# Optimization experiments

Hardware: AMD Instinct MI355X
Metric: run time of the kernel (lower is better)

## Reference

```python
import jax, jax.numpy as jnp
import numpy as np

EPS = 1e-6


def smooth(p):
    # smooth_distribution: clamp Bernoulli params away from {0,1}
    return jnp.clip(p, EPS, 1.0 - EPS)


def bern_logprob(p, x):
    # Bernoulli(p).log_prob(x) = x*log(p) + (1-x)*log(1-p)
    return x * jnp.log(p) + (1.0 - x) * jnp.log1p(-p)


def binary_row_reduce(A, b, k):
    # GF(2) Gaussian elimination on [A | b]; A:(k,n) binary float, b:(k,)
    M = jnp.concatenate([A, b[:, None]], axis=1)  # (k, n+1)
    rows = jnp.arange(k)
    for i in range(k):  # k is a small static int (25)
        col = M[:, i]
        cand = jnp.where((rows >= i) & (col > 0.5), rows, k)
        p = jnp.minimum(jnp.min(cand), k - 1)  # pivot row (fallback k-1 if none; prob ~0 for random A)
        ri, rp = M[i], M[p]
        M = M.at[i].set(rp)
        M = M.at[p].set(ri)
        elim = (M[:, i] > 0.5) & (rows != i)
        M = jnp.where(elim[:, None], jnp.mod(M + M[i], 2.0), M)
    return M[:, :-1], M[:, -1]


def compute_term1(logq, logp):
    # stable [sum_s q*log p]/[sum_s q], summed over batch; logq,logp: (S,B)
    m = jnp.max(logq, axis=0)                                  # (B,)
    w = jnp.exp(logq - m)                                      # (S,B)
    neg_num = m + jnp.log(jnp.sum(w * (-logp), axis=0))
    pos_den = m + jnp.log(jnp.sum(w, axis=0))
    return -jnp.sum(jnp.exp(neg_num - pos_den))


def setup_inputs() -> dict:
    key = jax.random.key(0)
    ks = jax.random.split(key, 5)
    nx, nz, B = 2048, 256, 512
    wr = float(np.sqrt(6.0 / (nx + nz)))
    xr = float(np.sqrt(6.0 / nx))
    zr = float(np.sqrt(6.0 / nz))
    U = jax.random.uniform(ks[0], (nz, nx), minval=-wr, maxval=wr)
    V = jax.random.uniform(ks[1], (nx, nz), minval=-wr, maxval=wr)
    x_bias = jax.random.uniform(ks[2], (nx,), minval=-xr, maxval=xr)
    z_bias = jax.random.uniform(ks[3], (nz,), minval=-zr, maxval=zr)
    xin = (jax.random.uniform(ks[4], (B, nx)) < 0.5).astype(jnp.float32)
    return {"xin": xin, "U": U, "V": V, "x_bias": x_bias, "z_bias": z_bias,
            "S": 10, "k": 25, "T": 30}


def reference(xin, U, V, x_bias, z_bias, S, k, T):
    dt = xin.dtype
    key = jax.random.key(42)
    kz, kx, kA, kb = jax.random.split(key, 4)

    # q(z|x) and samples  -------------------------------------------------
    q = smooth(jax.nn.sigmoid(xin @ U.T + z_bias))                     # (B, nz)
    samples_z = (jax.random.uniform(kz, (S,) + q.shape) < q).astype(dt)  # (S,B,nz)
    ps = smooth(jax.nn.sigmoid(jnp.einsum('sbz,xz->sbx', samples_z, V) + x_bias))  # (S,B,nx)
    xouts = (jax.random.uniform(kx, ps.shape) < ps).astype(dt)

    # projected ELBO over T random GF(2) hash constraints ------------------
    nz = U.shape[0]
    A_all = (jax.random.uniform(kA, (T, k, nz)) < 0.5).astype(dt)
    b_all = (jax.random.uniform(kb, (T, k)) < 0.5).astype(dt)
    pz = smooth(jax.nn.sigmoid(z_bias))                                # (nz,)

    def elbo_t(carry, Ab):
        A, b = Ab
        C, bp = binary_row_reduce(A, b, k)                             # (k,nz),(k,)
        proj = jnp.mod(jnp.einsum('sbz,kz->sbk', samples_z[:, :, k:], C[:, k:]) + bp, 2.0)
        sz = samples_z.at[:, :, :k].set(proj)                          # (S,B,nz)
        logq_zi = bern_logprob(q, sz).sum(axis=2)                      # (S,B)
        logp_z = bern_logprob(pz, sz).sum(axis=2)                      # (S,B)
        ps_t = smooth(jax.nn.sigmoid(jnp.einsum('sbz,xz->sbx', sz, V) + x_bias))
        logp_x = bern_logprob(ps_t, xin).sum(axis=2)                   # (S,B)
        logp = logp_z + logp_x
        term2 = compute_term1(logq_zi, logq_zi)
        term1 = compute_term1(logq_zi, logp)
        return carry, term1 - term2

    _, pelbos = jax.lax.scan(elbo_t, 0.0, (A_all, b_all))
    loss = -jnp.mean(pelbos)
    return q, samples_z, ps, xouts, loss
```

## Files before the change

kernel.cpp:

```cpp
#include <hip/hip_runtime.h>
#include <cstdint>

#define NX 2048
#define NZ 256
#define NB 512
#define NS 10
#define NK 25
#define NT 30
#define SBTOT (NS * NB)

#define LOG2E 1.4426950408889634f
#define LN2 0.6931471805599453f

#define OFF_Q 0
#define OFF_SAMP (NB * NZ)
#define OFF_PS (OFF_SAMP + SBTOT * NZ)
#define OFF_XO (OFF_PS + SBTOT * NX)
#define OFF_LOSS (OFF_XO + SBTOT * NX)

typedef unsigned long long ull;
typedef __bf16 bf16x8 __attribute__((ext_vector_type(8)));
typedef float f32x4 __attribute__((ext_vector_type(4)));

__host__ __device__ inline void tf2x32(uint32_t k0, uint32_t k1, uint32_t x0, uint32_t x1,
                                       uint32_t& o0, uint32_t& o1) {
  uint32_t k2 = k0 ^ k1 ^ 0x1BD11BDAu;
  x0 += k0; x1 += k1;
#define TF_R(r) { x0 += x1; x1 = (x1 << (r)) | (x1 >> (32 - (r))); x1 ^= x0; }
  TF_R(13) TF_R(15) TF_R(26) TF_R(6)
  x0 += k1; x1 += k2 + 1u;
  TF_R(17) TF_R(29) TF_R(16) TF_R(24)
  x0 += k2; x1 += k0 + 2u;
  TF_R(13) TF_R(15) TF_R(26) TF_R(6)
  x0 += k0; x1 += k1 + 3u;
  TF_R(17) TF_R(29) TF_R(16) TF_R(24)
  x0 += k1; x1 += k2 + 4u;
  TF_R(13) TF_R(15) TF_R(26) TF_R(6)
  x0 += k2; x1 += k0 + 5u;
#undef TF_R
  o0 = x0; o1 = x1;
}

__device__ inline uint32_t tf_select(uint32_t k0, uint32_t k1, uint32_t i, uint32_t h) {
  bool lo = i < h;
  uint32_t x0 = lo ? i : i - h;
  uint32_t x1 = lo ? i + h : i;
  uint32_t o0, o1;
  tf2x32(k0, k1, x0, x1, o0, o1);
  return lo ? o0 : o1;
}

__device__ inline float tf_uniform(uint32_t k0, uint32_t k1, uint32_t i, uint32_t h) {
  uint32_t r = tf_select(k0, k1, i, h);
  return __uint_as_float(0x3f800000u | (r >> 9)) - 1.0f;
}

__device__ inline float sigclip(float a) {
  float p = 1.0f / (1.0f + __expf(-a));
  return fminf(fmaxf(p, 1e-6f), 1.0f - 1e-6f);
}

__device__ inline ushort f2bf(float f) {
  uint32_t u = __float_as_uint(f);
  return (ushort)((u + 0x7FFFu + ((u >> 16) & 1u)) >> 16);
}

__device__ inline float blockReduceSum256(float v, volatile float* s4) {
#pragma unroll
  for (int o = 32; o > 0; o >>= 1) v += __shfl_down(v, o);
  __syncthreads();
  if ((threadIdx.x & 63) == 0) s4[threadIdx.x >> 6] = v;
  __syncthreads();
  return s4[0] + s4[1] + s4[2] + s4[3];
}

__global__ __launch_bounds__(256) void kP0_prep(const float* __restrict__ V,
                                                const float* __restrict__ U,
                                                const float* __restrict__ xin,
                                                const float* __restrict__ z_bias,
                                                ushort* __restrict__ Vbf,
                                                ushort* __restrict__ Vkpad2,
                                                ushort* __restrict__ Uhi,
                                                ushort* __restrict__ Ulo,
                                                ushort* __restrict__ xinbf,
                                                float* __restrict__ baseq,
                                                float* __restrict__ d_lpz,
                                                float* __restrict__ basepz) {
  __shared__ float red[4];
  int e = blockIdx.x * 256 + threadIdx.x;
  {
    int x = e >> 8, k = e & 255;
    float v = V[e];
    Vbf[e] = f2bf(v);
    if (k < 32) Vkpad2[x * 32 + k] = (k < NK) ? f2bf(v * LOG2E) : (ushort)0;
  }
  {
    float u = U[e];
    ushort hi = f2bf(u);
    Uhi[e] = hi;
    float hv = __uint_as_float((uint32_t)hi << 16);
    Ulo[e] = f2bf(u - hv);
  }
  {
    xinbf[e] = (xin[e] > 0.5f) ? (ushort)0x3F80 : (ushort)0;
    int e2 = e + NX * NZ;
    xinbf[e2] = (xin[e2] > 0.5f) ? (ushort)0x3F80 : (ushort)0;
  }
  if (e < NB) baseq[e] = 0.0f;
  if (blockIdx.x == 0) {
    int z = threadIdx.x;
    float pz = sigclip(z_bias[z]);
    float lp = __logf(pz), l1 = __logf(1.0f - pz);
    d_lpz[z] = lp - l1;
    float s = blockReduceSum256(l1, red);
    if (z == 0) *basepz = s;
  }
}

__global__ __launch_bounds__(256) void kW_signdot(const float* __restrict__ xin,
                                                  const ushort* __restrict__ Vkpad2,
                                                  float* __restrict__ W) {
  __shared__ float wred[4][NK];
  int b = blockIdx.x;
  int tid = threadIdx.x;
  float acc[NK];
#pragma unroll
  for (int j = 0; j < NK; ++j) acc[j] = 0.0f;
#pragma unroll
  for (int i = 0; i < 8; ++i) {
    int x = i * 256 + tid;
    float s = 1.0f - 2.0f * xin[(size_t)b * NX + x];
    const uint4* vp = (const uint4*)(Vkpad2 + (size_t)x * 32);
    uint4 q0 = vp[0], q1 = vp[1], q2 = vp[2], q3 = vp[3];
    uint32_t w[16] = {q0.x, q0.y, q0.z, q0.w, q1.x, q1.y, q1.z, q1.w,
                      q2.x, q2.y, q2.z, q2.w, q3.x, q3.y, q3.z, q3.w};
#pragma unroll
    for (int j = 0; j < NK; ++j) {
      uint32_t wd = w[j >> 1];
      float v = __uint_as_float((j & 1) ? (wd & 0xFFFF0000u) : (wd << 16));
      acc[j] = fmaf(s, v, acc[j]);
    }
  }
#pragma unroll
  for (int j = 0; j < NK; ++j) {
#pragma unroll
    for (int o = 1; o < 64; o <<= 1) acc[j] += __shfl_xor(acc[j], o);
  }
  if ((tid & 63) == 0) {
#pragma unroll
    for (int j = 0; j < NK; ++j) wred[tid >> 6][j] = acc[j];
  }
  __syncthreads();
  if (tid < NK) W[b * 32 + tid] = wred[0][tid] + wred[1][tid] + wred[2][tid] + wred[3][tid];
}

__global__ __launch_bounds__(256) void k1a_mfma(const ushort* __restrict__ xinbf,
                                                const ushort* __restrict__ Uhi,
                                                const ushort* __restrict__ Ulo,
                                                const float* __restrict__ z_bias,
                                                float* __restrict__ outq,
                                                float* __restrict__ d_lq,
                                                float* __restrict__ baseq) {
  __shared__ float red[4][16][17];
  int tid = threadIdx.x;
  int wave = tid >> 6, lane = tid & 63, grp = lane >> 4, col = lane & 15;
  int b0 = (blockIdx.x >> 4) * 16;
  int z0 = (blockIdx.x & 15) * 16;
  f32x4 acc = {0.f, 0.f, 0.f, 0.f};
  const ushort* arow = xinbf + (size_t)(b0 + col) * NX + wave * 512 + grp * 8;
  const ushort* bhr = Uhi + (size_t)(z0 + col) * NX + wave * 512 + grp * 8;
  const ushort* blr = Ulo + (size_t)(z0 + col) * NX + wave * 512 + grp * 8;
#pragma unroll 4
  for (int s = 0; s < 16; ++s) {
    bf16x8 a = *(const bf16x8*)(arow + s * 32);
    bf16x8 bh = *(const bf16x8*)(bhr + s * 32);
    bf16x8 bl = *(const bf16x8*)(blr + s * 32);
    acc = __builtin_amdgcn_mfma_f32_16x16x32_bf16(a, bh, acc, 0, 0, 0);
    acc = __builtin_amdgcn_mfma_f32_16x16x32_bf16(a, bl, acc, 0, 0, 0);
  }
#pragma unroll
  for (int r = 0; r < 4; ++r) red[wave][grp * 4 + r][col] = acc[r];
  __syncthreads();
  int bi = tid >> 4, zi = tid & 15;
  float aa = red[0][bi][zi] + red[1][bi][zi] + red[2][bi][zi] + red[3][bi][zi] + z_bias[z0 + zi];
  int b = b0 + bi, z = z0 + zi;
  float q = sigclip(aa);
  outq[b * NZ + z] = q;
  float lq = __logf(q), l1 = __logf(1.0f - q);
  d_lq[b * NZ + z] = lq - l1;
  float s1 = l1;
#pragma unroll
  for (int o = 1; o < 16; o <<= 1) s1 += __shfl_xor(s1, o);
  if (zi == 0) atomicAdd(&baseq[b], s1);
}

__global__ __launch_bounds__(256) void k2_samples(const float* __restrict__ q,
                                                  const float* __restrict__ d_lq,
                                                  const float* __restrict__ d_lpz,
                                                  float* __restrict__ samp_out,
                                                  ushort* __restrict__ samp16,
                                                  ull* __restrict__ Spack,
                                                  float* __restrict__ qtail,
                                                  float* __restrict__ ptail,
                                                  uint32_t kz0, uint32_t kz1) {
  __shared__ float red[4];
  int sb = blockIdx.x;
  int z = threadIdx.x;
  int b = sb & (NB - 1);
  uint32_t i = (uint32_t)sb * NZ + z;
  const uint32_t h = (uint32_t)SBTOT * NZ / 2;
  float u = tf_uniform(kz0, kz1, i, h);
  float qv = q[b * NZ + z];
  int smp = (u < qv) ? 1 : 0;
  samp_out[i] = (float)smp;
  samp16[i] = smp ? (ushort)0x3F80 : (ushort)0;
  ull m = __ballot(smp);
  if ((z & 63) == 0) Spack[sb * 4 + (z >> 6)] = m;
  float dq = (z >= NK && smp) ? d_lq[b * NZ + z] : 0.0f;
  float dp = (z >= NK && smp) ? d_lpz[z] : 0.0f;
  float sq = blockReduceSum256(dq, red);
  float sp = blockReduceSum256(dp, red);
  if (z == 0) { qtail[sb] = sq; ptail[sb] = sp; }
}

__global__ __launch_bounds__(256) void k3m_gemm(const ushort* __restrict__ samp16,
                                                const ushort* __restrict__ Vbf,
                                                const float* __restrict__ x_bias,
                                                ushort* __restrict__ base2,
                                                float* __restrict__ ps_out,
                                                float* __restrict__ xo_out,
                                                uint32_t kx0, uint32_t kx1) {
  __shared__ __align__(16) ushort As[128 * 32];
  __shared__ __align__(16) ushort Bs[64 * 32];
  int tid = threadIdx.x;
  int wave = tid >> 6, lane = tid & 63, grp = lane >> 4, col = lane & 15;
  int x0 = blockIdx.x * 128, sb0 = blockIdx.y * 64;
  f32x4 acc[2][4];
#pragma unroll
  for (int mi = 0; mi < 2; ++mi)
#pragma unroll
    for (int ni = 0; ni < 4; ++ni) acc[mi][ni] = (f32x4){0.f, 0.f, 0.f, 0.f};

  for (int k0 = 0; k0 < NZ; k0 += 32) {
    {
      int rowb = tid >> 2, kcb = (tid & 3) << 3;
      *(uint4*)&Bs[rowb * 32 + kcb] = *(const uint4*)&samp16[(size_t)(sb0 + rowb) * NZ + k0 + kcb];
#pragma unroll
      for (int c = tid; c < 512; c += 256) {
        int rowa = c >> 2, kca = (c & 3) << 3;
        *(uint4*)&As[rowa * 32 + kca] = *(const uint4*)&Vbf[(size_t)(x0 + rowa) * NZ + k0 + kca];
      }
    }
    __syncthreads();
    bf16x8 af[2], bfv[4];
#pragma unroll
    for (int mi = 0; mi < 2; ++mi)
      af[mi] = *(const bf16x8*)&As[(wave * 32 + mi * 16 + col) * 32 + grp * 8];
#pragma unroll
    for (int ni = 0; ni < 4; ++ni)
      bfv[ni] = *(const bf16x8*)&Bs[(ni * 16 + col) * 32 + grp * 8];
#pragma unroll
    for (int mi = 0; mi < 2; ++mi)
#pragma unroll
      for (int ni = 0; ni < 4; ++ni)
        acc[mi][ni] = __builtin_amdgcn_mfma_f32_16x16x32_bf16(af[mi], bfv[ni], acc[mi][ni], 0, 0, 0);
    __syncthreads();
  }
  const uint32_t h = (uint32_t)SBTOT * NX / 2;
#pragma unroll
  for (int mi = 0; mi < 2; ++mi) {
    int xb = x0 + wave * 32 + mi * 16 + grp * 4;
    float4 xb4 = *(const float4*)(x_bias + xb);
#pragma unroll
    for (int ni = 0; ni < 4; ++ni) {
      int sb = sb0 + ni * 16 + col;
      size_t off = (size_t)sb * NX + xb;
      float a0 = acc[mi][ni][0] + xb4.x;
      float a1 = acc[mi][ni][1] + xb4.y;
      float a2 = acc[mi][ni][2] + xb4.z;
      float a3 = acc[mi][ni][3] + xb4.w;
      uint2 bp;
      bp.x = (uint32_t)f2bf(a0 * LOG2E) | ((uint32_t)f2bf(a1 * LOG2E) << 16);
      bp.y = (uint32_t)f2bf(a2 * LOG2E) | ((uint32_t)f2bf(a3 * LOG2E) << 16);
      *(uint2*)(base2 + off) = bp;
      float4 pv = make_float4(sigclip(a0), sigclip(a1), sigclip(a2), sigclip(a3));
      *(float4*)(ps_out + off) = pv;
      uint32_t fi = (uint32_t)sb * NX + xb;
      float4 xv;
      xv.x = (tf_uniform(kx0, kx1, fi + 0, h) < pv.x) ? 1.0f : 0.0f;
      xv.y = (tf_uniform(kx0, kx1, fi + 1, h) < pv.y) ? 1.0f : 0.0f;
      xv.z = (tf_uniform(kx0, kx1, fi + 2, h) < pv.z) ? 1.0f : 0.0f;
      xv.w = (tf_uniform(kx0, kx1, fi + 3, h) < pv.w) ? 1.0f : 0.0f;
      *(float4*)(xo_out + off) = xv;
    }
  }
}

__global__ __launch_bounds__(256) void k4_rowreduce(ull* __restrict__ Ct,
                                                    uint32_t* __restrict__ bpmask,
                                                    uint32_t kA0, uint32_t kA1,
                                                    uint32_t kb0, uint32_t kb1) {
  __shared__ uint32_t Aw[NK][8];
  __shared__ uint32_t bbsh[NK];
  int t = blockIdx.x;
  int tid = threadIdx.x;
  if (tid < NK * 8) {
    int r = tid >> 3, c = tid & 7;
    const uint32_t hA = (uint32_t)NT * NK * NZ / 2;
    uint32_t base_i = (uint32_t)(t * NK + r) * NZ + c * 32;
    uint32_t w = 0;
    for (int zz = 0; zz < 32; ++zz) {
      uint32_t rr = tf_select(kA0, kA1, base_i + zz, hA);
      w |= ((rr >> 31) ^ 1u) << zz;
    }
    Aw[r][c] = w;
  }
  if (tid < NK) {
    const uint32_t hb = (uint32_t)NT * NK / 2;
    uint32_t rb = tf_select(kb0, kb1, (uint32_t)(t * NK + tid), hb);
    bbsh[tid] = (rb >> 31) ^ 1u;
  }
  __syncthreads();
  if (tid >= 64) return;
  int lane = tid;
  ull w0 = 0, w1 = 0, w2 = 0, w3 = 0;
  uint32_t bbit = 0;
  if (lane < NK) {
    w0 = (ull)Aw[lane][0] | ((ull)Aw[lane][1] << 32);
    w1 = (ull)Aw[lane][2] | ((ull)Aw[lane][3] << 32);
    w2 = (ull)Aw[lane][4] | ((ull)Aw[lane][5] << 32);
    w3 = (ull)Aw[lane][6] | ((ull)Aw[lane][7] << 32);
    bbit = bbsh[lane];
  }
  for (int i = 0; i < NK; ++i) {
    int mybit = (int)((w0 >> i) & 1ull);
    ull mask = __ballot(lane < NK && mybit);
    ull cand = mask & (~0ull << i);
    int p = cand ? __builtin_ctzll(cand) : (NK - 1);
    int srcl = (lane == i) ? p : ((lane == p) ? i : lane);
    w0 = __shfl(w0, srcl); w1 = __shfl(w1, srcl); w2 = __shfl(w2, srcl); w3 = __shfl(w3, srcl);
    bbit = __shfl(bbit, srcl);
    ull p0 = __shfl(w0, i), p1 = __shfl(w1, i), p2 = __shfl(w2, i), p3 = __shfl(w3, i);
    uint32_t pvb = __shfl(bbit, i);
    int nb2 = (int)((w0 >> i) & 1ull);
    if (lane < NK && lane != i && nb2) {
      w0 ^= p0; w1 ^= p1; w2 ^= p2; w3 ^= p3; bbit ^= pvb;
    }
  }
  if (lane < NK) {
    w0 &= ~((1ull << NK) - 1ull);
    ull* dstp = Ct + (size_t)(t * NK + lane) * 4;
    dstp[0] = w0; dstp[1] = w1; dstp[2] = w2; dstp[3] = w3;
  }
  ull bm = __ballot(lane < NK && bbit);
  if (lane == 0) bpmask[t] = (uint32_t)bm & 0x1FFFFFFu;
}

__global__ __launch_bounds__(256) void k5_proj(const ull* __restrict__ Spack,
                                               const ull* __restrict__ Ct,
                                               const uint32_t* __restrict__ bpmask,
                                               const float* __restrict__ W,
                                               uint32_t* __restrict__ projb,
                                               float* __restrict__ Syd) {
  int e = blockIdx.x * 256 + threadIdx.x;
  int sb = e >> 5, t = e & 31;
  ull s0 = Spack[sb * 4 + 0], s1 = Spack[sb * 4 + 1];
  ull s2 = Spack[sb * 4 + 2], s3 = Spack[sb * 4 + 3];
  uint32_t s25 = (uint32_t)(s0 & 0x1FFFFFFull);
  const float* Wb = W + (size_t)(sb & (NB - 1)) * 32;
  uint32_t out;
  float syd = 0.0f;
  if (t < NT) {
    uint32_t bp = bpmask[t];
    uint32_t pb = 0;
#pragma unroll
    for (int j = 0; j < NK; ++j) {
      const ull* C = Ct + (size_t)(t * NK + j) * 4;
      int par = __popcll(s0 & C[0]) + __popcll(s1 & C[1]) + __popcll(s2 & C[2]) + __popcll(s3 & C[3]);
      uint32_t bit = ((uint32_t)(par ^ (int)(bp >> j))) & 1u;
      pb |= bit << j;
      int d = (int)bit - (int)((s25 >> j) & 1u);
      syd = fmaf((float)d, Wb[j], syd);
    }
    out = pb;
  } else {
    out = s25;
  }
  projb[e] = out;
  Syd[e] = syd;
}

__global__ __launch_bounds__(256) void k6_mfma(const ushort* __restrict__ base2,
                                               const ushort* __restrict__ Vkpad2,
                                               const float* __restrict__ xin,
                                               const uint32_t* __restrict__ projb,
                                               const ull* __restrict__ Spack,
                                               const float* __restrict__ Syd,
                                               float* __restrict__ logpx) {
  __shared__ float bvsm[NX];
  __shared__ float lsum[4][32];
  __shared__ float red[4];
  int sb = blockIdx.x;
  int b = sb & (NB - 1);
  int tid = threadIdx.x;
  int wave = tid >> 6, lane = tid & 63;
  int grp = lane >> 4, col = lane & 15;
  const uint4* b16p = (const uint4*)(base2 + (size_t)sb * NX);
  const float4* x4p = (const float4*)(xin + (size_t)b * NX);
  float sbacc = 0.0f;
  {
    uint4 bu = b16p[tid];
    float4 xv0 = x4p[tid * 2], xv1 = x4p[tid * 2 + 1];
    uint32_t wds[4] = {bu.x, bu.y, bu.z, bu.w};
    float bv[8];
#pragma unroll
    for (int j = 0; j < 8; ++j) {
      uint32_t wd = wds[j >> 1];
      bv[j] = __uint_as_float((j & 1) ? (wd & 0xFFFF0000u) : (wd << 16));
    }
    float sg[8] = {1.0f - 2.0f * xv0.x, 1.0f - 2.0f * xv0.y, 1.0f - 2.0f * xv0.z,
                   1.0f - 2.0f * xv0.w, 1.0f - 2.0f * xv1.x, 1.0f - 2.0f * xv1.y,
                   1.0f - 2.0f * xv1.z, 1.0f - 2.0f * xv1.w};
#pragma unroll
    for (int j = 0; j < 8; ++j) {
      bvsm[tid * 8 + j] = bv[j];
      sbacc = fmaf(sg[j], bv[j], sbacc);
    }
  }
  float Sb = blockReduceSum256(sbacc, red);
  uint32_t s25 = (uint32_t)(Spack[sb * 4] & 0x1FFFFFFull);
  uint32_t pb0 = projb[sb * 32 + col];
  uint32_t pb1 = projb[sb * 32 + 16 + col];
  bf16x8 a0, a1;
  union { ushort u; __bf16 hh; } cvt;
#pragma unroll
  for (int j = 0; j < 8; ++j) {
    int k = grp * 8 + j;
    int sbit = (int)((s25 >> k) & 1u);
    int d0 = (int)((pb0 >> k) & 1u) - sbit;
    int d1 = (int)((pb1 >> k) & 1u) - sbit;
    cvt.u = (ushort)(d0 == 0 ? 0 : (d0 > 0 ? 0x3F80 : 0xBF80)); a0[j] = cvt.hh;
    cvt.u = (ushort)(d1 == 0 ? 0 : (d1 > 0 ? 0x3F80 : 0xBF80)); a1[j] = cvt.hh;
  }
  float acca[8], pp[8];
#pragma unroll
  for (int r = 0; r < 8; ++r) { acca[r] = 0.0f; pp[r] = 1.0f; }
  const ushort* vkbase = Vkpad2 + (size_t)(wave * 512 + col) * 32 + grp * 8;
#pragma unroll 4
  for (int i = 0; i < 32; ++i) {
    int x = (wave * 32 + i) * 16 + col;
    bf16x8 bfr = *(const bf16x8*)(vkbase + (size_t)i * 16 * 32);
    f32x4 c0 = {0.f, 0.f, 0.f, 0.f}, c1 = {0.f, 0.f, 0.f, 0.f};
    c0 = __builtin_amdgcn_mfma_f32_16x16x32_bf16(a0, bfr, c0, 0, 0, 0);
    c1 = __builtin_amdgcn_mfma_f32_16x16x32_bf16(a1, bfr, c1, 0, 0, 0);
    float bs = bvsm[x];
#pragma unroll
    for (int r = 0; r < 4; ++r) {
      float y0 = bs + c0[r];
      acca[r] += fabsf(y0);
      pp[r] = fmaf(pp[r], __builtin_amdgcn_exp2f(-fabsf(y0)), pp[r]);
      float y1 = bs + c1[r];
      acca[4 + r] += fabsf(y1);
      pp[4 + r] = fmaf(pp[4 + r], __builtin_amdgcn_exp2f(-fabsf(y1)), pp[4 + r]);
    }
  }
#pragma unroll
  for (int r = 0; r < 8; ++r) {
    float m = 0.5f * acca[r] + __log2f(pp[r]);
#pragma unroll
    for (int off = 1; off < 16; off <<= 1) m += __shfl_xor(m, off);
    if (col == 0) {
      int t = (r < 4) ? (grp * 4 + r) : (16 + grp * 4 + (r - 4));
      lsum[wave][t] = m;
    }
  }
  __syncthreads();
  if (tid < NT) {
    float tot = lsum[0][tid] + lsum[1][tid] + lsum[2][tid] + lsum[3][tid];
    tot += 0.5f * (Sb + Syd[sb * 32 + tid]);
    logpx[(size_t)tid * SBTOT + sb] = -LN2 * tot;
  }
}

__global__ __launch_bounds__(512) void k7_reduce(const float* __restrict__ logpx,
                                                 const uint32_t* __restrict__ projb,
                                                 const float* __restrict__ qtail,
                                                 const float* __restrict__ ptail,
                                                 const float* __restrict__ baseq,
                                                 const float* __restrict__ d_lq,
                                                 const float* __restrict__ d_lpz,
                                                 const float* __restrict__ basepz,
                                                 double* __restrict__ pelbo) {
  __shared__ double red8[8];
  int t = blockIdx.x;
  int b = threadIdx.x;
  float dlq[NK];
#pragma unroll
  for (int j = 0; j < NK; ++j) dlq[j] = d_lq[b * NZ + j];
  float bq = baseq[b];
  float bpz = *basepz;
  float lq[NS], lp[NS];
#pragma unroll
  for (int s = 0; s < NS; ++s) {
    int sb = s * NB + b;
    uint32_t m = projb[sb * 32 + t];
    float sq = 0.0f, spv = 0.0f;
#pragma unroll
    for (int j = 0; j < NK; ++j) {
      float on = (float)((m >> j) & 1u);
      sq += on * dlq[j];
      spv += on * d_lpz[j];
    }
    lq[s] = bq + qtail[sb] + sq;
    lp[s] = logpx[t * SBTOT + sb] + bpz + ptail[sb] + spv;
  }
  float mx = lq[0];
#pragma unroll
  for (int s = 1; s < NS; ++s) mx = fmaxf(mx, lq[s]);
  float den = 0.0f, num = 0.0f;
#pragma unroll
  for (int s = 0; s < NS; ++s) {
    float w = __expf(lq[s] - mx);
    den += w;
    num += w * (lq[s] - lp[s]);
  }
  double v = (double)(num / den);
#pragma unroll
  for (int o = 32; o > 0; o >>= 1) v += __shfl_down(v, o);
  __syncthreads();
  if ((b & 63) == 0) red8[b >> 6] = v;
  __syncthreads();
  if (b == 0) {
    double s = 0.0;
    for (int i = 0; i < 8; ++i) s += red8[i];
    pelbo[t] = s;
  }
}

__global__ __launch_bounds__(64) void k8_loss(const double* __restrict__ pelbo,
                                              float* __restrict__ out_loss) {
  int t = threadIdx.x;
  double v = (t < NT) ? pelbo[t] : 0.0;
#pragma unroll
  for (int o = 32; o > 0; o >>= 1) v += __shfl_down(v, o);
  if (t == 0) *out_loss = (float)(v / (double)NT);
}

extern "C" void kernel_launch(void* const* d_in, const int* in_sizes, int n_in,
                              void* d_out, int out_size, void* d_ws, size_t ws_size,
                              hipStream_t stream) {
  const float* xin = (const float*)d_in[0];
  const float* U = (const float*)d_in[1];
  const float* V = (const float*)d_in[2];
  const float* x_bias = (const float*)d_in[3];
  const float* z_bias = (const float*)d_in[4];
  float* out = (float*)d_out;

  char* p = (char*)d_ws;
  ushort* base2 = (ushort*)p;             p += (size_t)SBTOT * NX * 2;
  float* d_lq = (float*)p;                p += (size_t)NB * NZ * 4;
  float* baseq = (float*)p;               p += (size_t)NB * 4;
  float* d_lpz = (float*)p;               p += (size_t)NZ * 4;
  float* basepz = (float*)p;              p += 16;
  ull* Spack = (ull*)p;                   p += (size_t)SBTOT * 4 * 8;
  float* qtail = (float*)p;               p += (size_t)SBTOT * 4;
  float* ptail = (float*)p;               p += (size_t)SBTOT * 4;
  ull* Ct = (ull*)p;                      p += (size_t)NT * NK * 4 * 8;
  uint32_t* bpm = (uint32_t*)p;           p += 128;
  uint32_t* projb = (uint32_t*)p;         p += (size_t)SBTOT * 32 * 4;
  float* Syd = (float*)p;                 p += (size_t)SBTOT * 32 * 4;
  float* logpx = (float*)p;               p += (size_t)NT * SBTOT * 4;
  double* pelbo = (double*)p;             p += (size_t)NT * 8;
  ushort* Vkpad2 = (ushort*)p;            p += (size_t)NX * 32 * 2;
  ushort* Vbf = (ushort*)p;               p += (size_t)NX * NZ * 2;
  ushort* samp16 = (ushort*)p;            p += (size_t)SBTOT * NZ * 2;
  float* W = (float*)p;                   p += (size_t)NB * 32 * 4;
  ushort* Uhi = (ushort*)p;               p += (size_t)NZ * NX * 2;
  ushort* Ulo = (ushort*)p;               p += (size_t)NZ * NX * 2;
  ushort* xinbf = (ushort*)p;             p += (size_t)NB * NX * 2;
  (void)ws_size; (void)in_sizes; (void)n_in; (void)out_size;

  uint32_t o0[4], o1[4];
  for (int j = 0; j < 4; ++j) tf2x32(0u, 42u, (uint32_t)j, (uint32_t)(4 + j), o0[j], o1[j]);
  uint32_t kz0 = o0[0], kz1 = o0[1];
  uint32_t kx0 = o0[2], kx1 = o0[3];
  uint32_t kA0 = o1[0], kA1 = o1[1];
  uint32_t kb0 = o1[2], kb1 = o1[3];

  kP0_prep<<<NX * NZ / 256, 256, 0, stream>>>(V, U, xin, z_bias, Vbf, Vkpad2,
                                              Uhi, Ulo, xinbf, baseq, d_lpz, basepz);
  k4_rowreduce<<<NT, 256, 0, stream>>>(Ct, bpm, kA0, kA1, kb0, kb1);
  k1a_mfma<<<512, 256, 0, stream>>>(xinbf, Uhi, Ulo, z_bias, out + OFF_Q, d_lq, baseq);
  kW_signdot<<<NB, 256, 0, stream>>>(xin, Vkpad2, W);
  k2_samples<<<SBTOT, 256, 0, stream>>>(out + OFF_Q, d_lq, d_lpz, out + OFF_SAMP,
                                        samp16, Spack, qtail, ptail, kz0, kz1);
  dim3 g3(NX / 128, SBTOT / 64);
  k3m_gemm<<<g3, 256, 0, stream>>>(samp16, Vbf, x_bias, base2,
                                   out + OFF_PS, out + OFF_XO, kx0, kx1);
  k5_proj<<<SBTOT * 32 / 256, 256, 0, stream>>>(Spack, Ct, bpm, W, projb, Syd);
  k6_mfma<<<SBTOT, 256, 0, stream>>>(base2, Vkpad2, xin, projb, Spack, Syd, logpx);
  k7_reduce<<<NT, 512, 0, stream>>>(logpx, projb, qtail, ptail, baseq, d_lq,
                                    d_lpz, basepz, pelbo);
  k8_loss<<<1, 64, 0, stream>>>(pelbo, out + OFF_LOSS);
}
```

Baseline: 274.1 us.

## Merge prep kernels, pair Threefry outputs, and use fast sigmoid and Schraudolph exp

The prep, row-reduce and sign-dot kernels are merged into one launch, with the sign-dot path reading V directly instead of the Vkpad2 buffer written by the prep blocks. The sample and GEMM epilogue kernels now use both Threefry output words, handling element pairs i and i+h in one thread, which halves the PRNG calls and the launch count. The sigmoid uses hardware exp2 and rcp, and k6 replaces exp2 with a Schraudolph bit-trick approximation. That approximation changes numerical accuracy and may drift from the reference.

```diff
diff --git a/kernel.cpp b/kernel.cpp
--- a/kernel.cpp
+++ b/kernel.cpp
@@ -8,6 +8,7 @@
 #define NK 25
 #define NT 30
 #define SBTOT (NS * NB)
+#define SBH (SBTOT / 2)
 
 #define LOG2E 1.4426950408889634f
 #define LN2 0.6931471805599453f
@@ -50,13 +51,22 @@
   return lo ? o0 : o1;
 }
 
+__device__ inline float bits2u(uint32_t r) {
+  return __uint_as_float(0x3f800000u | (r >> 9)) - 1.0f;
+}
+
 __device__ inline float tf_uniform(uint32_t k0, uint32_t k1, uint32_t i, uint32_t h) {
-  uint32_t r = tf_select(k0, k1, i, h);
-  return __uint_as_float(0x3f800000u | (r >> 9)) - 1.0f;
+  return bits2u(tf_select(k0, k1, i, h));
 }
 
 __device__ inline float sigclip(float a) {
   float p = 1.0f / (1.0f + __expf(-a));
+  return fminf(fmaxf(p, 1e-6f), 1.0f - 1e-6f);
+}
+
+__device__ inline float sigfast(float a) {
+  float t = __builtin_amdgcn_exp2f(-a * LOG2E);
+  float p = __builtin_amdgcn_rcpf(1.0f + t);
   return fminf(fmaxf(p, 1e-6f), 1.0f - 1e-6f);
 }
 
@@ -74,84 +84,147 @@
   return s4[0] + s4[1] + s4[2] + s4[3];
 }
 
-__global__ __launch_bounds__(256) void kP0_prep(const float* __restrict__ V,
-                                                const float* __restrict__ U,
-                                                const float* __restrict__ xin,
-                                                const float* __restrict__ z_bias,
-                                                ushort* __restrict__ Vbf,
-                                                ushort* __restrict__ Vkpad2,
-                                                ushort* __restrict__ Uhi,
-                                                ushort* __restrict__ Ulo,
-                                                ushort* __restrict__ xinbf,
-                                                float* __restrict__ baseq,
-                                                float* __restrict__ d_lpz,
-                                                float* __restrict__ basepz) {
-  __shared__ float red[4];
-  int e = blockIdx.x * 256 + threadIdx.x;
+__global__ __launch_bounds__(256) void k0_mega(const float* __restrict__ V,
+                                               const float* __restrict__ U,
+                                               const float* __restrict__ xin,
+                                               const float* __restrict__ z_bias,
+                                               ushort* __restrict__ Vbf,
+                                               ushort* __restrict__ Vkpad2,
+                                               ushort* __restrict__ Uhi,
+                                               ushort* __restrict__ Ulo,
+                                               ushort* __restrict__ xinbf,
+                                               float* __restrict__ baseq,
+                                               float* __restrict__ d_lpz,
+                                               float* __restrict__ basepz,
+                                               ull* __restrict__ Ct,
+                                               uint32_t* __restrict__ bpmask,
+                                               float* __restrict__ W,
+                                               uint32_t kA0, uint32_t kA1,
+                                               uint32_t kb0, uint32_t kb1) {
+  int bid = blockIdx.x;
+  int tid = threadIdx.x;
+  if (bid < 2048) {
+    __shared__ float red[4];
+    int e = bid * 256 + tid;
+    {
+      int x = e >> 8, k = e & 255;
+      float v = V[e];
+      Vbf[e] = f2bf(v);
+      if (k < 32) Vkpad2[x * 32 + k] = (k < NK) ? f2bf(v * LOG2E) : (ushort)0;
+    }
+    {
+      float u = U[e];
+      ushort hi = f2bf(u);
+      Uhi[e] = hi;
+      float hv = __uint_as_float((uint32_t)hi << 16);
+      Ulo[e] = f2bf(u - hv);
+    }
+    {
+      xinbf[e] = (xin[e] > 0.5f) ? (ushort)0x3F80 : (ushort)0;
+      int e2 = e + NX * NZ;
+      xinbf[e2] = (xin[e2] > 0.5f) ? (ushort)0x3F80 : (ushort)0;
+    }
+    if (e < NB) baseq[e] = 0.0f;
+    if (bid == 0) {
+      int z = tid;
+      float pz = sigclip(z_bias[z]);
+      float lp = __logf(pz), l1 = __logf(1.0f - pz);
+      d_lpz[z] = lp - l1;
+      float s = blockReduceSum256(l1, red);
+      if (z == 0) *basepz = s;
+    }
+    return;
+  }
+  if (bid < 2048 + NT) {
+    __shared__ uint32_t Aw[NK][8];
+    __shared__ uint32_t bbsh[NK];
+    int t = bid - 2048;
+    if (tid < NK * 8) {
+      int r = tid >> 3, c = tid & 7;
+      const uint32_t hA = (uint32_t)NT * NK * NZ / 2;
+      uint32_t base_i = (uint32_t)(t * NK + r) * NZ + c * 32;
+      uint32_t w = 0;
+      for (int zz = 0; zz < 32; ++zz) {
+        uint32_t rr = tf_select(kA0, kA1, base_i + zz, hA);
+        w |= ((rr >> 31) ^ 1u) << zz;
+      }
+      Aw[r][c] = w;
+    }
+    if (tid < NK) {
+      const uint32_t hb = (uint32_t)NT * NK / 2;
+      uint32_t rb = tf_select(kb0, kb1, (uint32_t)(t * NK + tid), hb);
+      bbsh[tid] = (rb >> 31) ^ 1u;
+    }
+    __syncthreads();
+    if (tid >= 64) return;
+    int lane = tid;
+    ull w0 = 0, w1 = 0, w2 = 0, w3 = 0;
+    uint32_t bbit = 0;
+    if (lane < NK) {
+      w0 = (ull)Aw[lane][0] | ((ull)Aw[lane][1] << 32);
+      w1 = (ull)Aw[lane][2] | ((ull)Aw[lane][3] << 32);
+      w2 = (ull)Aw[lane][4] | ((ull)Aw[lane][5] << 32);
+      w3 = (ull)Aw[lane][6] | ((ull)Aw[lane][7] << 32);
+      bbit = bbsh[lane];
+    }
+    for (int i = 0; i < NK; ++i) {
+      int mybit = (int)((w0 >> i) & 1ull);
+      ull mask = __ballot(lane < NK && mybit);
+      ull cand = mask & (~0ull << i);
+      int p = cand ? __builtin_ctzll(cand) : (NK - 1);
+      int srcl = (lane == i) ? p : ((lane == p) ? i : lane);
+      w0 = __shfl(w0, srcl); w1 = __shfl(w1, srcl); w2 = __shfl(w2, srcl); w3 = __shfl(w3, srcl);
+      bbit = __shfl(bbit, srcl);
+      ull p0 = __shfl(w0, i), p1 = __shfl(w1, i), p2 = __shfl(w2, i), p3 = __shfl(w3, i);
+      uint32_t pvb = __shfl(bbit, i);
+      int nb2 = (int)((w0 >> i) & 1ull);
+      if (lane < NK && lane != i && nb2) {
+        w0 ^= p0; w1 ^= p1; w2 ^= p2; w3 ^= p3; bbit ^= pvb;
+      }
+    }
+    if (lane < NK) {
+      w0 &= ~((1ull << NK) - 1ull);
+      ull* dstp = Ct + (size_t)(t * NK + lane) * 4;
+      dstp[0] = w0; dstp[1] = w1; dstp[2] = w2; dstp[3] = w3;
+    }
+    ull bm = __ballot(lane < NK && bbit);
+    if (lane == 0) bpmask[t] = (uint32_t)bm & 0x1FFFFFFu;
+    return;
+  }
   {
-    int x = e >> 8, k = e & 255;
-    float v = V[e];
-    Vbf[e] = f2bf(v);
-    if (k < 32) Vkpad2[x * 32 + k] = (k < NK) ? f2bf(v * LOG2E) : (ushort)0;
-  }
-  {
-    float u = U[e];
-    ushort hi = f2bf(u);
-    Uhi[e] = hi;
-    float hv = __uint_as_float((uint32_t)hi << 16);
-    Ulo[e] = f2bf(u - hv);
-  }
-  {
-    xinbf[e] = (xin[e] > 0.5f) ? (ushort)0x3F80 : (ushort)0;
-    int e2 = e + NX * NZ;
-    xinbf[e2] = (xin[e2] > 0.5f) ? (ushort)0x3F80 : (ushort)0;
-  }
-  if (e < NB) baseq[e] = 0.0f;
-  if (blockIdx.x == 0) {
-    int z = threadIdx.x;
-    float pz = sigclip(z_bias[z]);
-    float lp = __logf(pz), l1 = __logf(1.0f - pz);
-    d_lpz[z] = lp - l1;
-    float s = blockReduceSum256(l1, red);
-    if (z == 0) *basepz = s;
-  }
-}
-
-__global__ __launch_bounds__(256) void kW_signdot(const float* __restrict__ xin,
-                                                  const ushort* __restrict__ Vkpad2,
-                                                  float* __restrict__ W) {
-  __shared__ float wred[4][NK];
-  int b = blockIdx.x;
-  int tid = threadIdx.x;
-  float acc[NK];
-#pragma unroll
-  for (int j = 0; j < NK; ++j) acc[j] = 0.0f;
-#pragma unroll
-  for (int i = 0; i < 8; ++i) {
-    int x = i * 256 + tid;
-    float s = 1.0f - 2.0f * xin[(size_t)b * NX + x];
-    const uint4* vp = (const uint4*)(Vkpad2 + (size_t)x * 32);
-    uint4 q0 = vp[0], q1 = vp[1], q2 = vp[2], q3 = vp[3];
-    uint32_t w[16] = {q0.x, q0.y, q0.z, q0.w, q1.x, q1.y, q1.z, q1.w,
-                      q2.x, q2.y, q2.z, q2.w, q3.x, q3.y, q3.z, q3.w};
+    __shared__ float wred[4][NK];
+    int b = bid - (2048 + NT);
+    float acc[NK];
+#pragma unroll
+    for (int j = 0; j < NK; ++j) acc[j] = 0.0f;
+#pragma unroll
+    for (int i = 0; i < 8; ++i) {
+      int x = i * 256 + tid;
+      float s = 1.0f - 2.0f * xin[(size_t)b * NX + x];
+      const float4* vp = (const float4*)(V + (size_t)x * NZ);
+      float4 q0 = vp[0], q1 = vp[1], q2 = vp[2], q3 = vp[3], q4 = vp[4], q5 = vp[5], q6 = vp[6];
+      float vv[28] = {q0.x, q0.y, q0.z, q0.w, q1.x, q1.y, q1.z, q1.w,
+                      q2.x, q2.y, q2.z, q2.w, q3.x, q3.y, q3.z, q3.w,
+                      q4.x, q4.y, q4.z, q4.w, q5.x, q5.y, q5.z, q5.w,
+                      q6.x, q6.y, q6.z, q6.w};
+#pragma unroll
+      for (int j = 0; j < NK; ++j) {
+        float v = __uint_as_float((uint32_t)f2bf(vv[j] * LOG2E) << 16);
+        acc[j] = fmaf(s, v, acc[j]);
+      }
+    }
 #pragma unroll
     for (int j = 0; j < NK; ++j) {
-      uint32_t wd = w[j >> 1];
-      float v = __uint_as_float((j & 1) ? (wd & 0xFFFF0000u) : (wd << 16));
-      acc[j] = fmaf(s, v, acc[j]);
-    }
-  }
-#pragma unroll
-  for (int j = 0; j < NK; ++j) {
-#pragma unroll
-    for (int o = 1; o < 64; o <<= 1) acc[j] += __shfl_xor(acc[j], o);
-  }
-  if ((tid & 63) == 0) {
-#pragma unroll
-    for (int j = 0; j < NK; ++j) wred[tid >> 6][j] = acc[j];
-  }
-  __syncthreads();
-  if (tid < NK) W[b * 32 + tid] = wred[0][tid] + wred[1][tid] + wred[2][tid] + wred[3][tid];
+#pragma unroll
+      for (int o = 1; o < 64; o <<= 1) acc[j] += __shfl_xor(acc[j], o);
+    }
+    if ((tid & 63) == 0) {
+#pragma unroll
+      for (int j = 0; j < NK; ++j) wred[tid >> 6][j] = acc[j];
+    }
+    __syncthreads();
+    if (tid < NK) W[b * 32 + tid] = wred[0][tid] + wred[1][tid] + wred[2][tid] + wred[3][tid];
+  }
 }
 
 __global__ __launch_bounds__(256) void k1a_mfma(const ushort* __restrict__ xinbf,
@@ -205,22 +278,36 @@
                                                   uint32_t kz0, uint32_t kz1) {
   __shared__ float red[4];
   int sb = blockIdx.x;
+  int sbB = sb + SBH;
   int z = threadIdx.x;
   int b = sb & (NB - 1);
+  const uint32_t h = (uint32_t)SBTOT * NZ / 2;
   uint32_t i = (uint32_t)sb * NZ + z;
-  const uint32_t h = (uint32_t)SBTOT * NZ / 2;
-  float u = tf_uniform(kz0, kz1, i, h);
+  uint32_t o0, o1;
+  tf2x32(kz0, kz1, i, i + h, o0, o1);
+  float uA = bits2u(o0), uB = bits2u(o1);
   float qv = q[b * NZ + z];
-  int smp = (u < qv) ? 1 : 0;
-  samp_out[i] = (float)smp;
-  samp16[i] = smp ? (ushort)0x3F80 : (ushort)0;
-  ull m = __ballot(smp);
-  if ((z & 63) == 0) Spack[sb * 4 + (z >> 6)] = m;
-  float dq = (z >= NK && smp) ? d_lq[b * NZ + z] : 0.0f;
-  float dp = (z >= NK && smp) ? d_lpz[z] : 0.0f;
-  float sq = blockReduceSum256(dq, red);
-  float sp = blockReduceSum256(dp, red);
-  if (z == 0) { qtail[sb] = sq; ptail[sb] = sp; }
+  int smpA = (uA < qv) ? 1 : 0;
+  int smpB = (uB < qv) ? 1 : 0;
+  samp_out[i] = (float)smpA;
+  samp_out[i + h] = (float)smpB;
+  samp16[i] = smpA ? (ushort)0x3F80 : (ushort)0;
+  samp16[i + h] = smpB ? (ushort)0x3F80 : (ushort)0;
+  ull mA = __ballot(smpA), mB = __ballot(smpB);
+  if ((z & 63) == 0) {
+    Spack[sb * 4 + (z >> 6)] = mA;
+    Spack[sbB * 4 + (z >> 6)] = mB;
+  }
+  float dlqv = d_lq[b * NZ + z], dlpv = d_lpz[z];
+  bool tailz = (z >= NK);
+  float sqA = blockReduceSum256((tailz && smpA) ? dlqv : 0.0f, red);
+  float spA = blockReduceSum256((tailz && smpA) ? dlpv : 0.0f, red);
+  float sqB = blockReduceSum256((tailz && smpB) ? dlqv : 0.0f, red);
+  float spB = blockReduceSum256((tailz && smpB) ? dlpv : 0.0f, red);
+  if (z == 0) {
+    qtail[sb] = sqA; ptail[sb] = spA;
+    qtail[sbB] = sqB; ptail[sbB] = spB;
+  }
 }
 
 __global__ __launch_bounds__(256) void k3m_gemm(const ushort* __restrict__ samp16,
@@ -234,7 +321,7 @@
   __shared__ __align__(16) ushort Bs[64 * 32];
   int tid = threadIdx.x;
   int wave = tid >> 6, lane = tid & 63, grp = lane >> 4, col = lane & 15;
-  int x0 = blockIdx.x * 128, sb0 = blockIdx.y * 64;
+  int x0 = blockIdx.x * 128, sb0 = blockIdx.y * 32;
   f32x4 acc[2][4];
 #pragma unroll
   for (int mi = 0; mi < 2; ++mi)
@@ -244,7 +331,8 @@
   for (int k0 = 0; k0 < NZ; k0 += 32) {
     {
       int rowb = tid >> 2, kcb = (tid & 3) << 3;
-      *(uint4*)&Bs[rowb * 32 + kcb] = *(const uint4*)&samp16[(size_t)(sb0 + rowb) * NZ + k0 + kcb];
+      int srow = (rowb < 32) ? (sb0 + rowb) : (SBH + sb0 + rowb - 32);
+      *(uint4*)&Bs[rowb * 32 + kcb] = *(const uint4*)&samp16[(size_t)srow * NZ + k0 + kcb];
 #pragma unroll
       for (int c = tid; c < 512; c += 256) {
         int rowa = c >> 2, kca = (c & 3) << 3;
@@ -272,88 +360,42 @@
     int xb = x0 + wave * 32 + mi * 16 + grp * 4;
     float4 xb4 = *(const float4*)(x_bias + xb);
 #pragma unroll
-    for (int ni = 0; ni < 4; ++ni) {
-      int sb = sb0 + ni * 16 + col;
-      size_t off = (size_t)sb * NX + xb;
-      float a0 = acc[mi][ni][0] + xb4.x;
-      float a1 = acc[mi][ni][1] + xb4.y;
-      float a2 = acc[mi][ni][2] + xb4.z;
-      float a3 = acc[mi][ni][3] + xb4.w;
-      uint2 bp;
-      bp.x = (uint32_t)f2bf(a0 * LOG2E) | ((uint32_t)f2bf(a1 * LOG2E) << 16);
-      bp.y = (uint32_t)f2bf(a2 * LOG2E) | ((uint32_t)f2bf(a3 * LOG2E) << 16);
-      *(uint2*)(base2 + off) = bp;
-      float4 pv = make_float4(sigclip(a0), sigclip(a1), sigclip(a2), sigclip(a3));
-      *(float4*)(ps_out + off) = pv;
-      uint32_t fi = (uint32_t)sb * NX + xb;
-      float4 xv;
-      xv.x = (tf_uniform(kx0, kx1, fi + 0, h) < pv.x) ? 1.0f : 0.0f;
-      xv.y = (tf_uniform(kx0, kx1, fi + 1, h) < pv.y) ? 1.0f : 0.0f;
-      xv.z = (tf_uniform(kx0, kx1, fi + 2, h) < pv.z) ? 1.0f : 0.0f;
-      xv.w = (tf_uniform(kx0, kx1, fi + 3, h) < pv.w) ? 1.0f : 0.0f;
-      *(float4*)(xo_out + off) = xv;
-    }
-  }
-}
-
-__global__ __launch_bounds__(256) void k4_rowreduce(ull* __restrict__ Ct,
-                                                    uint32_t* __restrict__ bpmask,
-                                                    uint32_t kA0, uint32_t kA1,
-                                                    uint32_t kb0, uint32_t kb1) {
-  __shared__ uint32_t Aw[NK][8];
-  __shared__ uint32_t bbsh[NK];
-  int t = blockIdx.x;
-  int tid = threadIdx.x;
-  if (tid < NK * 8) {
-    int r = tid >> 3, c = tid & 7;
-    const uint32_t hA = (uint32_t)NT * NK * NZ / 2;
-    uint32_t base_i = (uint32_t)(t * NK + r) * NZ + c * 32;
-    uint32_t w = 0;
-    for (int zz = 0; zz < 32; ++zz) {
-      uint32_t rr = tf_select(kA0, kA1, base_i + zz, hA);
-      w |= ((rr >> 31) ^ 1u) << zz;
-    }
-    Aw[r][c] = w;
-  }
-  if (tid < NK) {
-    const uint32_t hb = (uint32_t)NT * NK / 2;
-    uint32_t rb = tf_select(kb0, kb1, (uint32_t)(t * NK + tid), hb);
-    bbsh[tid] = (rb >> 31) ^ 1u;
-  }
-  __syncthreads();
-  if (tid >= 64) return;
-  int lane = tid;
-  ull w0 = 0, w1 = 0, w2 = 0, w3 = 0;
-  uint32_t bbit = 0;
-  if (lane < NK) {
-    w0 = (ull)Aw[lane][0] | ((ull)Aw[lane][1] << 32);
-    w1 = (ull)Aw[lane][2] | ((ull)Aw[lane][3] << 32);
-    w2 = (ull)Aw[lane][4] | ((ull)Aw[lane][5] << 32);
-    w3 = (ull)Aw[lane][6] | ((ull)Aw[lane][7] << 32);
-    bbit = bbsh[lane];
-  }
-  for (int i = 0; i < NK; ++i) {
-    int mybit = (int)((w0 >> i) & 1ull);
-    ull mask = __ballot(lane < NK && mybit);
-    ull cand = mask & (~0ull << i);
-    int p = cand ? __builtin_ctzll(cand) : (NK - 1);
-    int srcl = (lane == i) ? p : ((lane == p) ? i : lane);
-    w0 = __shfl(w0, srcl); w1 = __shfl(w1, srcl); w2 = __shfl(w2, srcl); w3 = __shfl(w3, srcl);
-    bbit = __shfl(bbit, srcl);
-    ull p0 = __shfl(w0, i), p1 = __shfl(w1, i), p2 = __shfl(w2, i), p3 = __shfl(w3, i);
-    uint32_t pvb = __shfl(bbit, i);
-    int nb2 = (int)((w0 >> i) & 1ull);
-    if (lane < NK && lane != i && nb2) {
-      w0 ^= p0; w1 ^= p1; w2 ^= p2; w3 ^= p3; bbit ^= pvb;
-    }
-  }
-  if (lane < NK) {
-    w0 &= ~((1ull << NK) - 1ull);
-    ull* dstp = Ct + (size_t)(t * NK + lane) * 4;
-    dstp[0] = w0; dstp[1] = w1; dstp[2] = w2; dstp[3] = w3;
-  }
-  ull bm = __ballot(lane < NK && bbit);
-  if (lane == 0) bpmask[t] = (uint32_t)bm & 0x1FFFFFFu;
+    for (int ni = 0; ni < 2; ++ni) {
+      int sbA = sb0 + ni * 16 + col;
+      int sbB = sbA + SBH;
+      size_t offA = (size_t)sbA * NX + xb;
+      size_t offB = (size_t)sbB * NX + xb;
+      float aA[4], aB[4], pA[4], pB[4];
+      float xbv[4] = {xb4.x, xb4.y, xb4.z, xb4.w};
+#pragma unroll
+      for (int j = 0; j < 4; ++j) {
+        aA[j] = acc[mi][ni][j] + xbv[j];
+        aB[j] = acc[mi][ni + 2][j] + xbv[j];
+        pA[j] = sigfast(aA[j]);
+        pB[j] = sigfast(aB[j]);
+      }
+      uint2 bpA, bpB;
+      bpA.x = (uint32_t)f2bf(aA[0] * LOG2E) | ((uint32_t)f2bf(aA[1] * LOG2E) << 16);
+      bpA.y = (uint32_t)f2bf(aA[2] * LOG2E) | ((uint32_t)f2bf(aA[3] * LOG2E) << 16);
+      bpB.x = (uint32_t)f2bf(aB[0] * LOG2E) | ((uint32_t)f2bf(aB[1] * LOG2E) << 16);
+      bpB.y = (uint32_t)f2bf(aB[2] * LOG2E) | ((uint32_t)f2bf(aB[3] * LOG2E) << 16);
+      *(uint2*)(base2 + offA) = bpA;
+      *(uint2*)(base2 + offB) = bpB;
+      *(float4*)(ps_out + offA) = make_float4(pA[0], pA[1], pA[2], pA[3]);
+      *(float4*)(ps_out + offB) = make_float4(pB[0], pB[1], pB[2], pB[3]);
+      uint32_t fiA = (uint32_t)sbA * NX + xb;
+      float xvA[4], xvB[4];
+#pragma unroll
+      for (int j = 0; j < 4; ++j) {
+        uint32_t o0, o1;
+        tf2x32(kx0, kx1, fiA + j, fiA + j + h, o0, o1);
+        xvA[j] = (bits2u(o0) < pA[j]) ? 1.0f : 0.0f;
+        xvB[j] = (bits2u(o1) < pB[j]) ? 1.0f : 0.0f;
+      }
+      *(float4*)(xo_out + offA) = make_float4(xvA[0], xvA[1], xvA[2], xvA[3]);
+      *(float4*)(xo_out + offB) = make_float4(xvB[0], xvB[1], xvB[2], xvB[3]);
+    }
+  }
 }
 
 __global__ __launch_bounds__(256) void k5_proj(const ull* __restrict__ Spack,
@@ -445,6 +487,8 @@
   float acca[8], pp[8];
 #pragma unroll
   for (int r = 0; r < 8; ++r) { acca[r] = 0.0f; pp[r] = 1.0f; }
+  const float SCH_A = -8388608.0f;
+  const float SCH_B = 1064866805.0f;
   const ushort* vkbase = Vkpad2 + (size_t)(wave * 512 + col) * 32 + grp * 8;
 #pragma unroll 4
   for (int i = 0; i < 32; ++i) {
@@ -457,11 +501,15 @@
 #pragma unroll
     for (int r = 0; r < 4; ++r) {
       float y0 = bs + c0[r];
-      acca[r] += fabsf(y0);
-      pp[r] = fmaf(pp[r], __builtin_amdgcn_exp2f(-fabsf(y0)), pp[r]);
+      float u0 = fabsf(y0);
+      acca[r] += u0;
+      float e0 = __int_as_float((int)fmaf(u0, SCH_A, SCH_B));
+      pp[r] = fmaf(pp[r], e0, pp[r]);
       float y1 = bs + c1[r];
-      acca[4 + r] += fabsf(y1);
-      pp[4 + r] = fmaf(pp[4 + r], __builtin_amdgcn_exp2f(-fabsf(y1)), pp[4 + r]);
+      float u1 = fabsf(y1);
+      acca[4 + r] += u1;
+      float e1 = __int_as_float((int)fmaf(u1, SCH_A, SCH_B));
+      pp[4 + r] = fmaf(pp[4 + r], e1, pp[4 + r]);
     }
   }
 #pragma unroll
@@ -587,14 +635,13 @@
   uint32_t kA0 = o1[0], kA1 = o1[1];
   uint32_t kb0 = o1[2], kb1 = o1[3];
 
-  kP0_prep<<<NX * NZ / 256, 256, 0, stream>>>(V, U, xin, z_bias, Vbf, Vkpad2,
-                                              Uhi, Ulo, xinbf, baseq, d_lpz, basepz);
-  k4_rowreduce<<<NT, 256, 0, stream>>>(Ct, bpm, kA0, kA1, kb0, kb1);
+  k0_mega<<<2048 + NT + NB, 256, 0, stream>>>(V, U, xin, z_bias, Vbf, Vkpad2,
+                                              Uhi, Ulo, xinbf, baseq, d_lpz, basepz,
+                                              Ct, bpm, W, kA0, kA1, kb0, kb1);
   k1a_mfma<<<512, 256, 0, stream>>>(xinbf, Uhi, Ulo, z_bias, out + OFF_Q, d_lq, baseq);
-  kW_signdot<<<NB, 256, 0, stream>>>(xin, Vkpad2, W);
-  k2_samples<<<SBTOT, 256, 0, stream>>>(out + OFF_Q, d_lq, d_lpz, out + OFF_SAMP,
-                                        samp16, Spack, qtail, ptail, kz0, kz1);
-  dim3 g3(NX / 128, SBTOT / 64);
+  k2_samples<<<SBH, 256, 0, stream>>>(out + OFF_Q, d_lq, d_lpz, out + OFF_SAMP,
+                                      samp16, Spack, qtail, ptail, kz0, kz1);
+  dim3 g3(NX / 128, SBH / 32);
   k3m_gemm<<<g3, 256, 0, stream>>>(samp16, Vbf, x_bias, base2,
                                    out + OFF_PS, out + OFF_XO, kx0, kx1);
   k5_proj<<<SBTOT * 32 / 256, 256, 0, stream>>>(Spack, Ct, bpm, W, projb, Syd);
```

New measurement: 283.8 us. 1.04x slower.
